# Performance work log

Hardware: AMD Instinct MI355X
Metric: run time of the kernel (lower is better)

## Reference

```python
import jax, jax.numpy as jnp
import numpy as np

B, S, H = 8, 1024, 1024
NH, HD = 16, 64
LN_EPS = 1e-12


def setup_inputs() -> dict:
    key = jax.random.key(0)
    ks = jax.random.split(key, 8)
    sd = 0.02
    return {
        "hidden_states": jax.random.normal(ks[0], (B, S, H), jnp.float32),
        "attention_mask": jnp.zeros((B, 1, 1, S), jnp.float32),
        "Wq": jax.random.normal(ks[1], (H, H), jnp.float32) * sd,
        "bq": jnp.zeros((H,), jnp.float32),
        "Wk": jax.random.normal(ks[2], (H, H), jnp.float32) * sd,
        "bk": jnp.zeros((H,), jnp.float32),
        "Wv": jax.random.normal(ks[3], (H, H), jnp.float32) * sd,
        "bv": jnp.zeros((H,), jnp.float32),
        "Wo": jax.random.normal(ks[4], (H, H), jnp.float32) * sd,
        "bo": jnp.zeros((H,), jnp.float32),
        "ln_gamma": jnp.ones((H,), jnp.float32),
        "ln_beta": jnp.zeros((H,), jnp.float32),
    }


def _heads(x):
    # [B,S,H] -> [B,NH,S,HD]
    return x.reshape(B, S, NH, HD).transpose(0, 2, 1, 3)


def reference(hidden_states, attention_mask, Wq, bq, Wk, bk, Wv, bv, Wo, bo, ln_gamma, ln_beta):
    # QKV projections (torch Linear: x @ W.T + b)
    q = _heads(hidden_states @ Wq.T + bq)
    k = _heads(hidden_states @ Wk.T + bk)
    v = _heads(hidden_states @ Wv.T + bv)
    # scaled dot-product attention with additive mask
    scores = jnp.einsum("bhqd,bhkd->bhqk", q, k) / np.sqrt(HD).astype(np.float32)
    scores = scores + attention_mask  # broadcast [B,1,1,S]
    probs = jax.nn.softmax(scores, axis=-1)
    ctx = jnp.einsum("bhqk,bhkd->bhqd", probs, v)
    ctx = ctx.transpose(0, 2, 1, 3).reshape(B, S, H)
    # output projection + residual + LayerNorm
    out = ctx @ Wo.T + bo
    x = out + hidden_states
    mu = jnp.mean(x, axis=-1, keepdims=True)
    var = jnp.var(x, axis=-1, keepdims=True)
    return (x - mu) * jax.lax.rsqrt(var + LN_EPS) * ln_gamma + ln_beta
```

## Files before the change

### kernel.cpp

```cpp
#include <hip/hip_runtime.h>
#include <stdint.h>

typedef __attribute__((ext_vector_type(8))) __bf16 bf16x8;
typedef __attribute__((ext_vector_type(8))) unsigned short ushortx8;
typedef __attribute__((ext_vector_type(4))) unsigned short ushortx4;
typedef __attribute__((ext_vector_type(4))) short short4v;
typedef __attribute__((ext_vector_type(4))) float floatx4;

#define ASYNC16(g, l) __builtin_amdgcn_global_load_lds( \
    (__attribute__((address_space(1))) void*)(g),       \
    (__attribute__((address_space(3))) void*)(l), 16, 0, 0)

__device__ __forceinline__ unsigned short f2bf(float f) {
    unsigned int u = __float_as_uint(f);
    u += 0x7fffu + ((u >> 16) & 1u);
    return (unsigned short)(u >> 16);
}

__device__ __forceinline__ floatx4 mfma32(bf16x8 a, bf16x8 b, floatx4 c) {
    return __builtin_amdgcn_mfma_f32_16x16x32_bf16(a, b, c, 0, 0, 0);
}
__device__ __forceinline__ floatx4 mfma16(short4v a, short4v b, floatx4 c) {
    return __builtin_amdgcn_mfma_f32_16x16x16bf16_1k(a, b, c, 0, 0, 0);
}

__global__ __launch_bounds__(256) void cvt_bf16(const float* __restrict__ in,
                                                unsigned short* __restrict__ out,
                                                int n8) {
    int i = blockIdx.x * 256 + threadIdx.x;
    if (i >= n8) return;
    const float4* p = (const float4*)in + (size_t)i * 2;
    float4 a = p[0], b = p[1];
    ushortx8 o;
    o[0] = f2bf(a.x); o[1] = f2bf(a.y); o[2] = f2bf(a.z); o[3] = f2bf(a.w);
    o[4] = f2bf(b.x); o[5] = f2bf(b.y); o[6] = f2bf(b.z); o[7] = f2bf(b.w);
    *((ushortx8*)out + i) = o;
}

__global__ __launch_bounds__(256) void cvt_w(const float* __restrict__ Wq,
                                             const float* __restrict__ Wk,
                                             const float* __restrict__ Wv,
                                             const float* __restrict__ Wo,
                                             unsigned short* __restrict__ oqkv,
                                             unsigned short* __restrict__ oo) {
    int blk = blockIdx.x >> 9;
    const float* src = (blk == 0) ? Wq : (blk == 1) ? Wk : (blk == 2) ? Wv : Wo;
    unsigned short* dst = (blk == 3) ? oo : oqkv + (size_t)blk * 1048576;
    int i = (blockIdx.x & 511) * 256 + threadIdx.x;
    const float4* p = (const float4*)src + (size_t)i * 2;
    float4 a = p[0], b = p[1];
    ushortx8 o;
    o[0] = f2bf(a.x); o[1] = f2bf(a.y); o[2] = f2bf(a.z); o[3] = f2bf(a.w);
    o[4] = f2bf(b.x); o[5] = f2bf(b.y); o[6] = f2bf(b.z); o[7] = f2bf(b.w);
    *((ushortx8*)dst + i) = o;
}

template<bool SWAP>
__device__ __forceinline__ void kloop_bk64(
    const unsigned short* __restrict__ Ag,
    const unsigned short* __restrict__ Wg,
    unsigned short* As, unsigned short* Bs,
    int wm, int wn, int l16, int quad, int t,
    floatx4 acc[4][4])
{
#pragma unroll 1
    for (int k0 = 0; k0 < 1024; k0 += 64) {
        __syncthreads();
#pragma unroll
        for (int i = 0; i < 4; i++) {
            ASYNC16(Ag + (size_t)i * 32 * 1024 + k0, As + i * 2048 + t * 8);
            ASYNC16(Wg + (size_t)i * 32 * 1024 + k0, Bs + i * 2048 + t * 8);
        }
        __syncthreads();
#pragma unroll
        for (int s = 0; s < 2; s++) {
            int pb = ((s * 4 + quad) ^ (l16 & 7)) * 8;
            bf16x8 af[4], bfr[4];
#pragma unroll
            for (int mt = 0; mt < 4; mt++)
                af[mt] = *(const bf16x8*)(As + (wm + mt * 16 + l16) * 64 + pb);
#pragma unroll
            for (int nt = 0; nt < 4; nt++)
                bfr[nt] = *(const bf16x8*)(Bs + (wn + nt * 16 + l16) * 64 + pb);
            if (SWAP) {
#pragma unroll
                for (int ft = 0; ft < 4; ft++)
#pragma unroll
                    for (int st = 0; st < 4; st++)
                        acc[ft][st] = mfma32(bfr[ft], af[st], acc[ft][st]);
            } else {
#pragma unroll
                for (int mt = 0; mt < 4; mt++)
#pragma unroll
                    for (int nt = 0; nt < 4; nt++)
                        acc[mt][nt] = mfma32(af[mt], bfr[nt], acc[mt][nt]);
            }
        }
    }
}

__global__ __launch_bounds__(256) void gemm_qkv(
    const unsigned short* __restrict__ A,
    const unsigned short* __restrict__ W,
    const float* __restrict__ bq, const float* __restrict__ bk, const float* __restrict__ bv,
    unsigned short* __restrict__ Qo, unsigned short* __restrict__ Ko,
    unsigned short* __restrict__ Vo)
{
    __shared__ unsigned short As[128 * 64];
    __shared__ unsigned short Bs[128 * 64];
    const int t = threadIdx.x;
    const int wave = t >> 6, lane = t & 63;
    const int quad = lane >> 4, l16 = lane & 15;
    const int wm = (wave >> 1) * 64, wn = (wave & 1) * 64;
    const int srow = t >> 3;
    const int scol = ((t & 7) ^ (srow & 7)) * 8;

    const unsigned short* Ag = A + ((size_t)blockIdx.x * 128 + srow) * 1024 + scol;
    const unsigned short* Wg = W + ((size_t)blockIdx.y * 128 + srow) * 1024 + scol;

    floatx4 acc[4][4] = {};
    kloop_bk64<true>(Ag, Wg, As, Bs, wm, wn, l16, quad, t, acc);

    int y = blockIdx.y;
    if (y < 16) {
        const float* bp = (y < 8) ? bq : bk;
        unsigned short* op = (y < 8) ? Qo : Ko;
#pragma unroll
        for (int ft = 0; ft < 4; ft++) {
            int featg = (y * 128 + wn + ft * 16 + quad * 4) & 1023;
            float4 b4 = *(const float4*)(bp + featg);
            int h = featg >> 6, d = featg & 63;
#pragma unroll
            for (int st = 0; st < 4; st++) {
                int sg = blockIdx.x * 128 + wm + st * 16 + l16;
                int b = sg >> 10, s = sg & 1023;
                ushortx4 o4;
                o4[0] = f2bf(acc[ft][st][0] + b4.x);
                o4[1] = f2bf(acc[ft][st][1] + b4.y);
                o4[2] = f2bf(acc[ft][st][2] + b4.z);
                o4[3] = f2bf(acc[ft][st][3] + b4.w);
                *(ushortx4*)(op + (((size_t)(b * 16 + h) * 1024 + s) * 64 + d)) = o4;
            }
        }
    } else {
#pragma unroll
        for (int ft = 0; ft < 4; ft++) {
            int featg = (y * 128 + wn + ft * 16 + quad * 4) & 1023;
            float4 b4 = *(const float4*)(bv + featg);
#pragma unroll
            for (int r = 0; r < 4; r++) {
                int feat = featg + r;
                int h = feat >> 6, d = feat & 63;
                float bias = (r == 0) ? b4.x : (r == 1) ? b4.y : (r == 2) ? b4.z : b4.w;
#pragma unroll
                for (int st = 0; st < 4; st++) {
                    int sg = blockIdx.x * 128 + wm + st * 16 + l16;
                    int b = sg >> 10, s = sg & 1023;
                    Vo[((size_t)(b * 16 + h) * 64 + d) * 1024 + s] = f2bf(acc[ft][st][r] + bias);
                }
            }
        }
    }
}

__global__ __launch_bounds__(256) void attn(
    const unsigned short* __restrict__ Q,
    const unsigned short* __restrict__ Kg,
    const unsigned short* __restrict__ Vt,
    const float* __restrict__ mask,
    unsigned short* __restrict__ ctx)
{
    __shared__ unsigned short Qs[128 * 64];
    __shared__ unsigned short Ks[64 * 64];
    __shared__ unsigned short Vs[64 * 64];
    __shared__ float Msall[1024];

    const int t = threadIdx.x;
    const int wave = t >> 6, lane = t & 63, quad = lane >> 4, l16 = lane & 15;
    const int s7 = l16 & 7;
    const int head = blockIdx.y;
    const int b = head >> 4, h = head & 15;
    const int q0 = blockIdx.x * 128;
    const unsigned short* Qh = Q + (size_t)head * 65536;
    const unsigned short* Kh = Kg + (size_t)head * 65536;
    const unsigned short* Vh = Vt + (size_t)head * 65536;

    const int srow = t >> 3;
    const int scol = ((t & 7) ^ (srow & 7)) * 8;

    *(float4*)(Msall + t * 4) = *(const float4*)(mask + b * 1024 + t * 4);

#pragma unroll
    for (int i = 0; i < 4; i++)
        ASYNC16(Qh + (size_t)(q0 + i * 32 + srow) * 64 + scol, Qs + i * 2048 + t * 8);
    __syncthreads();

    bf16x8 qf[2][2];
#pragma unroll
    for (int qg = 0; qg < 2; qg++) {
        int qrow = wave * 32 + qg * 16 + l16;
#pragma unroll
        for (int s = 0; s < 2; s++)
            qf[qg][s] = *(const bf16x8*)(Qs + qrow * 64 + (((s * 4 + quad) ^ s7) * 8));
    }

    float rs_acc[2] = {0.f, 0.f};
    floatx4 o_acc[2][4] = {};

    for (int k0 = 0; k0 < 1024; k0 += 64) {
        __syncthreads();
#pragma unroll
        for (int i = 0; i < 2; i++) {
            ASYNC16(Kh + (size_t)(k0 + i * 32 + srow) * 64 + scol, Ks + i * 2048 + t * 8);
            ASYNC16(Vh + (size_t)(i * 32 + srow) * 1024 + k0 + scol, Vs + i * 2048 + t * 8);
        }
        __syncthreads();

        bf16x8 kf[4][2];
#pragma unroll
        for (int nt = 0; nt < 4; nt++) {
            int krow = nt * 16 + l16;
#pragma unroll
            for (int s = 0; s < 2; s++)
                kf[nt][s] = *(const bf16x8*)(Ks + krow * 64 + (((s * 4 + quad) ^ s7) * 8));
        }

        short4v pf[2][4];
#pragma unroll
        for (int qg = 0; qg < 2; qg++) {
#pragma unroll
            for (int nt = 0; nt < 4; nt++) {
                floatx4 z = {0.f, 0.f, 0.f, 0.f};
                z = mfma32(kf[nt][0], qf[qg][0], z);
                z = mfma32(kf[nt][1], qf[qg][1], z);
                floatx4 mk = *(const floatx4*)(Msall + k0 + nt * 16 + quad * 4);
#pragma unroll
                for (int r = 0; r < 4; r++) {
                    float p = __expf(z[r] * 0.125f + mk[r]);
                    rs_acc[qg] += p;
                    pf[qg][nt][r] = (short)(__float_as_uint(p) >> 16);
                }
            }
        }

#pragma unroll
        for (int dt = 0; dt < 4; dt++) {
            int vrow = dt * 16 + l16;
#pragma unroll
            for (int nt = 0; nt < 4; nt++) {
                short4v vf = *(const short4v*)(Vs + vrow * 64 +
                                (((2 * nt + (quad >> 1)) ^ s7) * 8) + (quad & 1) * 4);
                o_acc[0][dt] = mfma16(vf, pf[0][nt], o_acc[0][dt]);
                o_acc[1][dt] = mfma16(vf, pf[1][nt], o_acc[1][dt]);
            }
        }
    }

#pragma unroll
    for (int qg = 0; qg < 2; qg++) {
        float v = rs_acc[qg];
        v += __shfl_xor(v, 16);
        v += __shfl_xor(v, 32);
        float inv_l = 1.0f / v;
        int qg_row = q0 + wave * 32 + qg * 16 + l16;
#pragma unroll
        for (int dt = 0; dt < 4; dt++) {
            ushortx4 o4;
#pragma unroll
            for (int r = 0; r < 4; r++) o4[r] = f2bf(o_acc[qg][dt][r] * inv_l);
            *(ushortx4*)(ctx + ((size_t)(b * 1024 + qg_row)) * 1024 + h * 64 + dt * 16 + quad * 4) = o4;
        }
    }
}

__global__ __launch_bounds__(256) void gemm_proj(
    const unsigned short* __restrict__ A,
    const unsigned short* __restrict__ W,
    const float* __restrict__ bo,
    const float* __restrict__ resid,
    float* __restrict__ X)
{
    __shared__ unsigned short As[128 * 64];
    __shared__ unsigned short Bs[128 * 64];
    const int t = threadIdx.x;
    const int wave = t >> 6, lane = t & 63;
    const int quad = lane >> 4, l16 = lane & 15;
    const int wm = (wave >> 1) * 64, wn = (wave & 1) * 64;
    const int srow = t >> 3;
    const int scol = ((t & 7) ^ (srow & 7)) * 8;

    const unsigned short* Ag = A + ((size_t)blockIdx.x * 128 + srow) * 1024 + scol;
    const unsigned short* Wg = W + ((size_t)blockIdx.y * 128 + srow) * 1024 + scol;

    floatx4 acc[4][4] = {};
    kloop_bk64<false>(Ag, Wg, As, Bs, wm, wn, l16, quad, t, acc);

#pragma unroll
    for (int nt = 0; nt < 4; nt++) {
        int gn = blockIdx.y * 128 + wn + nt * 16 + l16;
        float bias = bo[gn];
#pragma unroll
        for (int mt = 0; mt < 4; mt++) {
#pragma unroll
            for (int r = 0; r < 4; r++) {
                int gm = blockIdx.x * 128 + wm + mt * 16 + quad * 4 + r;
                size_t off = (size_t)gm * 1024 + gn;
                X[off] = acc[mt][nt][r] + bias + resid[off];
            }
        }
    }
}

__global__ __launch_bounds__(256) void ln_k(const float* __restrict__ X,
                                            const float* __restrict__ g,
                                            const float* __restrict__ be,
                                            float* __restrict__ out)
{
    int row = blockIdx.x;
    int t = threadIdx.x;
    const float* xr = X + (size_t)row * 1024;
    float4 v = *(const float4*)(xr + t * 4);
    float s = v.x + v.y + v.z + v.w;
    float ss = v.x * v.x + v.y * v.y + v.z * v.z + v.w * v.w;
    for (int off = 1; off < 64; off <<= 1) {
        s += __shfl_xor(s, off);
        ss += __shfl_xor(ss, off);
    }
    __shared__ float red[8];
    int wave = t >> 6, lane = t & 63;
    if (lane == 0) { red[wave] = s; red[4 + wave] = ss; }
    __syncthreads();
    s = red[0] + red[1] + red[2] + red[3];
    ss = red[4] + red[5] + red[6] + red[7];
    float mu = s * (1.f / 1024.f);
    float var = ss * (1.f / 1024.f) - mu * mu;
    float inv = rsqrtf(var + 1e-12f);
    float4 gv = *(const float4*)(g + t * 4);
    float4 bv = *(const float4*)(be + t * 4);
    float4 o;
    o.x = (v.x - mu) * inv * gv.x + bv.x;
    o.y = (v.y - mu) * inv * gv.y + bv.y;
    o.z = (v.z - mu) * inv * gv.z + bv.z;
    o.w = (v.w - mu) * inv * gv.w + bv.w;
    *(float4*)(out + (size_t)row * 1024 + t * 4) = o;
}

extern "C" void kernel_launch(void* const* d_in, const int* in_sizes, int n_in,
                              void* d_out, int out_size, void* d_ws, size_t ws_size,
                              hipStream_t stream)
{
    const float* hidden = (const float*)d_in[0];
    const float* mask   = (const float*)d_in[1];
    const float* Wq = (const float*)d_in[2];
    const float* bq = (const float*)d_in[3];
    const float* Wk = (const float*)d_in[4];
    const float* bk = (const float*)d_in[5];
    const float* Wv = (const float*)d_in[6];
    const float* bv = (const float*)d_in[7];
    const float* Wo = (const float*)d_in[8];
    const float* bo = (const float*)d_in[9];
    const float* gamma = (const float*)d_in[10];
    const float* beta  = (const float*)d_in[11];
    float* out = (float*)d_out;

    char* ws = (char*)d_ws;
    unsigned short* hid_bf  = (unsigned short*)(ws + 0);
    unsigned short* wqkv_bf = (unsigned short*)(ws + 16777216);
    unsigned short* wo_bf   = (unsigned short*)(ws + 23068672);
    unsigned short* vt_bf   = (unsigned short*)(ws + 25165824);
    unsigned short* ctx_bf  = (unsigned short*)(ws + 41943040);
    unsigned short* q_bf    = (unsigned short*)(ws + 58720256);
    unsigned short* k_bf    = (unsigned short*)(ws + 75497472);
    float* x_f = (float*)(ws + 58720256);

    cvt_bf16<<<4096, 256, 0, stream>>>(hidden, hid_bf, 1048576);
    cvt_w<<<2048, 256, 0, stream>>>(Wq, Wk, Wv, Wo, wqkv_bf, wo_bf);

    gemm_qkv<<<dim3(64, 24), 256, 0, stream>>>(hid_bf, wqkv_bf, bq, bk, bv, q_bf, k_bf, vt_bf);
    attn<<<dim3(8, 128), 256, 0, stream>>>(q_bf, k_bf, vt_bf, mask, ctx_bf);
    gemm_proj<<<dim3(64, 8), 256, 0, stream>>>(ctx_bf, wo_bf, bo, hidden, x_f);
    ln_k<<<8192, 256, 0, stream>>>(x_f, gamma, beta, out);
}
```

Baseline: 275.5 us.

## Fold softmax scale into Q, use exp2, MFMA row sums, permuted V layout

Several changes to the attention path. Q is prescaled by log2(e)/sqrt(d) in the QKV epilogue, and the mask is prescaled by log2(e), so the softmax can use exp2 with no per-element multiply. Row sums are now accumulated by an MFMA against a ones vector instead of scalar adds plus cross-lane shuffles. V^T is stored with a permuted sequence order so each V fragment comes from two 16-byte LDS loads instead of four 8-byte ones. The two conversion kernels are also merged into one launch; the V permutation has to match the attention read exactly, and rounding Q to bf16 after scaling slightly changes numerics.

New measurement: 288.8 us. 1.05x slower.

```diff
diff --git a/kernel.cpp b/kernel.cpp
--- a/kernel.cpp
+++ b/kernel.cpp
@@ -7,6 +7,9 @@
 typedef __attribute__((ext_vector_type(4))) short short4v;
 typedef __attribute__((ext_vector_type(4))) float floatx4;
 
+#define LOG2E 1.4426950408889634f
+#define QSCALE 0.18033688011112043f
+
 #define ASYNC16(g, l) __builtin_amdgcn_global_load_lds( \
     (__attribute__((address_space(1))) void*)(g),       \
     (__attribute__((address_space(3))) void*)(l), 16, 0, 0)
@@ -24,29 +27,25 @@
     return __builtin_amdgcn_mfma_f32_16x16x16bf16_1k(a, b, c, 0, 0, 0);
 }
 
-__global__ __launch_bounds__(256) void cvt_bf16(const float* __restrict__ in,
-                                                unsigned short* __restrict__ out,
-                                                int n8) {
-    int i = blockIdx.x * 256 + threadIdx.x;
-    if (i >= n8) return;
-    const float4* p = (const float4*)in + (size_t)i * 2;
-    float4 a = p[0], b = p[1];
-    ushortx8 o;
-    o[0] = f2bf(a.x); o[1] = f2bf(a.y); o[2] = f2bf(a.z); o[3] = f2bf(a.w);
-    o[4] = f2bf(b.x); o[5] = f2bf(b.y); o[6] = f2bf(b.z); o[7] = f2bf(b.w);
-    *((ushortx8*)out + i) = o;
-}
-
-__global__ __launch_bounds__(256) void cvt_w(const float* __restrict__ Wq,
-                                             const float* __restrict__ Wk,
-                                             const float* __restrict__ Wv,
-                                             const float* __restrict__ Wo,
-                                             unsigned short* __restrict__ oqkv,
-                                             unsigned short* __restrict__ oo) {
-    int blk = blockIdx.x >> 9;
-    const float* src = (blk == 0) ? Wq : (blk == 1) ? Wk : (blk == 2) ? Wv : Wo;
-    unsigned short* dst = (blk == 3) ? oo : oqkv + (size_t)blk * 1048576;
-    int i = (blockIdx.x & 511) * 256 + threadIdx.x;
+__global__ __launch_bounds__(256) void cvt_all(
+    const float* __restrict__ hidden,
+    const float* __restrict__ Wq, const float* __restrict__ Wk,
+    const float* __restrict__ Wv, const float* __restrict__ Wo,
+    unsigned short* __restrict__ hid_bf,
+    unsigned short* __restrict__ oqkv, unsigned short* __restrict__ oo)
+{
+    const float* src;
+    unsigned short* dst;
+    int i;
+    if (blockIdx.x < 4096) {
+        src = hidden; dst = hid_bf;
+        i = blockIdx.x * 256 + threadIdx.x;
+    } else {
+        int blk = (blockIdx.x - 4096) >> 9;
+        src = (blk == 0) ? Wq : (blk == 1) ? Wk : (blk == 2) ? Wv : Wo;
+        dst = (blk == 3) ? oo : oqkv + (size_t)blk * 1048576;
+        i = ((blockIdx.x - 4096) & 511) * 256 + threadIdx.x;
+    }
     const float4* p = (const float4*)src + (size_t)i * 2;
     float4 a = p[0], b = p[1];
     ushortx8 o;
@@ -125,6 +124,7 @@
     if (y < 16) {
         const float* bp = (y < 8) ? bq : bk;
         unsigned short* op = (y < 8) ? Qo : Ko;
+        float sc = (y < 8) ? QSCALE : 1.0f;
 #pragma unroll
         for (int ft = 0; ft < 4; ft++) {
             int featg = (y * 128 + wn + ft * 16 + quad * 4) & 1023;
@@ -135,10 +135,10 @@
                 int sg = blockIdx.x * 128 + wm + st * 16 + l16;
                 int b = sg >> 10, s = sg & 1023;
                 ushortx4 o4;
-                o4[0] = f2bf(acc[ft][st][0] + b4.x);
-                o4[1] = f2bf(acc[ft][st][1] + b4.y);
-                o4[2] = f2bf(acc[ft][st][2] + b4.z);
-                o4[3] = f2bf(acc[ft][st][3] + b4.w);
+                o4[0] = f2bf((acc[ft][st][0] + b4.x) * sc);
+                o4[1] = f2bf((acc[ft][st][1] + b4.y) * sc);
+                o4[2] = f2bf((acc[ft][st][2] + b4.z) * sc);
+                o4[3] = f2bf((acc[ft][st][3] + b4.w) * sc);
                 *(ushortx4*)(op + (((size_t)(b * 16 + h) * 1024 + s) * 64 + d)) = o4;
             }
         }
@@ -156,7 +156,8 @@
                 for (int st = 0; st < 4; st++) {
                     int sg = blockIdx.x * 128 + wm + st * 16 + l16;
                     int b = sg >> 10, s = sg & 1023;
-                    Vo[((size_t)(b * 16 + h) * 64 + d) * 1024 + s] = f2bf(acc[ft][st][r] + bias);
+                    int sp = (s & ~63) + (st >> 1) * 32 + (l16 >> 2) * 8 + (st & 1) * 4 + (l16 & 3);
+                    Vo[((size_t)(b * 16 + h) * 64 + d) * 1024 + sp] = f2bf(acc[ft][st][r] + bias);
                 }
             }
         }
@@ -188,7 +189,11 @@
     const int srow = t >> 3;
     const int scol = ((t & 7) ^ (srow & 7)) * 8;
 
-    *(float4*)(Msall + t * 4) = *(const float4*)(mask + b * 1024 + t * 4);
+    {
+        float4 m4 = *(const float4*)(mask + b * 1024 + t * 4);
+        m4.x *= LOG2E; m4.y *= LOG2E; m4.z *= LOG2E; m4.w *= LOG2E;
+        *(float4*)(Msall + t * 4) = m4;
+    }
 
 #pragma unroll
     for (int i = 0; i < 4; i++)
@@ -204,7 +209,8 @@
             qf[qg][s] = *(const bf16x8*)(Qs + qrow * 64 + (((s * 4 + quad) ^ s7) * 8));
     }
 
-    float rs_acc[2] = {0.f, 0.f};
+    const short4v ones = {(short)0x3F80, (short)0x3F80, (short)0x3F80, (short)0x3F80};
+    floatx4 acc_l[2] = {};
     floatx4 o_acc[2][4] = {};
 
     for (int k0 = 0; k0 < 1024; k0 += 64) {
@@ -217,12 +223,14 @@
         __syncthreads();
 
         bf16x8 kf[4][2];
+        floatx4 mk[4];
 #pragma unroll
         for (int nt = 0; nt < 4; nt++) {
             int krow = nt * 16 + l16;
 #pragma unroll
             for (int s = 0; s < 2; s++)
                 kf[nt][s] = *(const bf16x8*)(Ks + krow * 64 + (((s * 4 + quad) ^ s7) * 8));
+            mk[nt] = *(const floatx4*)(Msall + k0 + nt * 16 + quad * 4);
         }
 
         short4v pf[2][4];
@@ -233,35 +241,42 @@
                 floatx4 z = {0.f, 0.f, 0.f, 0.f};
                 z = mfma32(kf[nt][0], qf[qg][0], z);
                 z = mfma32(kf[nt][1], qf[qg][1], z);
-                floatx4 mk = *(const floatx4*)(Msall + k0 + nt * 16 + quad * 4);
 #pragma unroll
                 for (int r = 0; r < 4; r++) {
-                    float p = __expf(z[r] * 0.125f + mk[r]);
-                    rs_acc[qg] += p;
+                    float p = exp2f(z[r] + mk[nt][r]);
                     pf[qg][nt][r] = (short)(__float_as_uint(p) >> 16);
                 }
             }
         }
 
 #pragma unroll
+        for (int nt = 0; nt < 4; nt++) {
+            acc_l[0] = mfma16(ones, pf[0][nt], acc_l[0]);
+            acc_l[1] = mfma16(ones, pf[1][nt], acc_l[1]);
+        }
+
+#pragma unroll
         for (int dt = 0; dt < 4; dt++) {
             int vrow = dt * 16 + l16;
-#pragma unroll
-            for (int nt = 0; nt < 4; nt++) {
-                short4v vf = *(const short4v*)(Vs + vrow * 64 +
-                                (((2 * nt + (quad >> 1)) ^ s7) * 8) + (quad & 1) * 4);
-                o_acc[0][dt] = mfma16(vf, pf[0][nt], o_acc[0][dt]);
-                o_acc[1][dt] = mfma16(vf, pf[1][nt], o_acc[1][dt]);
+            ushortx8 v01 = *(const ushortx8*)(Vs + vrow * 64 + ((quad ^ s7) * 8));
+            ushortx8 v23 = *(const ushortx8*)(Vs + vrow * 64 + (((quad + 4) ^ s7) * 8));
+            short4v vf0 = {(short)v01[0], (short)v01[1], (short)v01[2], (short)v01[3]};
+            short4v vf1 = {(short)v01[4], (short)v01[5], (short)v01[6], (short)v01[7]};
+            short4v vf2 = {(short)v23[0], (short)v23[1], (short)v23[2], (short)v23[3]};
+            short4v vf3 = {(short)v23[4], (short)v23[5], (short)v23[6], (short)v23[7]};
+#pragma unroll
+            for (int qg = 0; qg < 2; qg++) {
+                o_acc[qg][dt] = mfma16(vf0, pf[qg][0], o_acc[qg][dt]);
+                o_acc[qg][dt] = mfma16(vf1, pf[qg][1], o_acc[qg][dt]);
+                o_acc[qg][dt] = mfma16(vf2, pf[qg][2], o_acc[qg][dt]);
+                o_acc[qg][dt] = mfma16(vf3, pf[qg][3], o_acc[qg][dt]);
             }
         }
     }
 
 #pragma unroll
     for (int qg = 0; qg < 2; qg++) {
-        float v = rs_acc[qg];
-        v += __shfl_xor(v, 16);
-        v += __shfl_xor(v, 32);
-        float inv_l = 1.0f / v;
+        float inv_l = 1.0f / acc_l[qg][0];
         int qg_row = q0 + wave * 32 + qg * 16 + l16;
 #pragma unroll
         for (int dt = 0; dt < 4; dt++) {
@@ -373,8 +388,7 @@
     unsigned short* k_bf    = (unsigned short*)(ws + 75497472);
     float* x_f = (float*)(ws + 58720256);
 
-    cvt_bf16<<<4096, 256, 0, stream>>>(hidden, hid_bf, 1048576);
-    cvt_w<<<2048, 256, 0, stream>>>(Wq, Wk, Wv, Wo, wqkv_bf, wo_bf);
+    cvt_all<<<6144, 256, 0, stream>>>(hidden, Wq, Wk, Wv, Wo, hid_bf, wqkv_bf, wo_bf);
 
     gemm_qkv<<<dim3(64, 24), 256, 0, stream>>>(hid_bf, wqkv_bf, bq, bk, bv, q_bf, k_bf, vt_bf);
     attn<<<dim3(8, 128), 256, 0, stream>>>(q_bf, k_bf, vt_bf, mask, ctx_bf);
```
